# Kernel tuning notes

Hardware: AMD Instinct MI355X
Metric: run time of the kernel (lower is better)

Reference implementation:

```python
import jax, jax.numpy as jnp
import numpy as np

B = 2048          # graphs in dense batch
NPG = 64          # nodes per graph (molecules are small)
N = B * NPG       # 131072 total nodes
E = 524288        # directed edges, avg degree 4
D = 275           # dim_inner
L = 5             # layers_mp
NF = 9            # atom categorical features
V = 128           # per-feature vocab
BN_EPS = 1e-5


def setup_inputs() -> dict:
    key = jax.random.key(0)
    ks = jax.random.split(key, 8)
    return {
        "x_atoms": jax.random.randint(ks[0], (N, NF), 0, 119, dtype=jnp.int64),
        "edge_index": jax.random.randint(ks[1], (2, E), 0, N, dtype=jnp.int64),
        "atom_emb": jax.random.normal(ks[2], (NF, V, D), jnp.float32) * 0.1,
        "conv_W": jax.random.normal(ks[3], (L, D, D), jnp.float32) * (1.0 / np.sqrt(D)),
        "conv_b": jnp.zeros((L, D), jnp.float32),
        "bn_gamma": jnp.ones((L, D), jnp.float32),
        "bn_beta": jnp.zeros((L, D), jnp.float32),
        "post_W": jax.random.normal(ks[4], (D, D), jnp.float32) * (1.0 / np.sqrt(D)),
        "post_b": jnp.zeros((D,), jnp.float32),
    }


def reference(x_atoms, edge_index, atom_emb, conv_W, conv_b, bn_gamma, bn_beta, post_W, post_b):
    n = x_atoms.shape[0]
    # AtomEncoder: sum of per-feature embedding lookups -> [N, D]
    h = jax.vmap(lambda tab, idx: tab[idx], in_axes=(0, 1))(atom_emb, x_atoms).sum(0)

    # GCN normalization with self loops (shared across layers since graph is fixed)
    loops = jnp.arange(n, dtype=edge_index.dtype)
    row = jnp.concatenate([edge_index[0], loops])  # source
    col = jnp.concatenate([edge_index[1], loops])  # target (aggregation index)
    deg = jax.ops.segment_sum(jnp.ones_like(row, h.dtype), col, num_segments=n)
    dinv = jnp.where(deg > 0, jax.lax.rsqrt(jnp.maximum(deg, 1e-12)), 0.0)
    norm = dinv[row] * dinv[col]  # [E+N]

    for i in range(L):
        xw = h @ conv_W[i].T                                   # [N, D] linear (no bias yet)
        msg = norm[:, None] * xw[row]                          # gather + edge scaling
        agg = jax.ops.segment_sum(msg, col, num_segments=n) + conv_b[i]
        # BatchNorm1d (training-mode batch stats, biased variance)
        mu = agg.mean(axis=0)
        var = agg.var(axis=0)
        hbn = (agg - mu) * jax.lax.rsqrt(var + BN_EPS) * bn_gamma[i] + bn_beta[i]
        h = jax.nn.relu(hbn)

    # post_mp: single Linear (MLPNoAct, num_layers=1)
    h = h @ post_W.T + post_b

    # graph_preprocess -> dense batch [B, NPG, D], then pairwise dot-product decode
    hd = h.reshape(B, NPG, D)
    logits = jnp.einsum('bnd,bmd->bnm', hd, hd)[..., None]     # [B, NPG, NPG, 1]
    return logits
```

## Files before the change

kernel.cpp:

```cpp
#include <hip/hip_runtime.h>
#include <hip/hip_bf16.h>
#include <cstdint>

#define NN 131072
#define NE 524288
#define DIM 275
#define DP 288
#define NFEAT 9
#define NVOC 128
#define NLAY 5
#define NPG 64
#define NGRAPH 2048
#define BN_EPS 1e-5f
#define BK 32
#define NEPAD (NE + 3 * NN)
#define LDSE 1536

typedef unsigned short u16;
typedef __attribute__((ext_vector_type(8))) short s16x8;
typedef __attribute__((ext_vector_type(4))) float f32x4;

#define GLL16(g, l) __builtin_amdgcn_global_load_lds( \
    (const __attribute__((address_space(1))) unsigned int*)(g), \
    (__attribute__((address_space(3))) unsigned int*)(l), 16, 0, 0)

__device__ __forceinline__ float bf2f(u16 u) {
  union { unsigned int i; float f; } x; x.i = ((unsigned int)u) << 16; return x.f;
}
__device__ __forceinline__ u16 f2bf(float f) {
  union { float f; unsigned int i; } x; x.f = f;
  unsigned int r = x.i + 0x7fffu + ((x.i >> 16) & 1u);
  return (u16)(r >> 16);
}
__device__ __forceinline__ void acc4(float* a, uint2 m) {
  a[0] += bf2f((u16)m.x); a[1] += bf2f((u16)(m.x >> 16));
  a[2] += bf2f((u16)m.y); a[3] += bf2f((u16)(m.y >> 16));
}


__global__ void hist_kernel(const int* __restrict__ ei, int* __restrict__ cnt) {
  int e = blockIdx.x * 256 + threadIdx.x;
  if (e < NE) atomicAdd(&cnt[ei[NE + e]], 1);
}

__global__ void pad_dinv_kernel(const int* __restrict__ cnt, int* __restrict__ cnt_pad,
                                float* __restrict__ dinv) {
  int v = blockIdx.x * 256 + threadIdx.x;
  if (v < NN) {
    int c = cnt[v];
    cnt_pad[v] = (c + 3) & ~3;
    dinv[v] = rsqrtf(1.0f + (float)c);
  }
}

__global__ void scan_block_kernel(const int* __restrict__ in, int* __restrict__ out_ex,
                                  int* __restrict__ partials) {
  __shared__ int buf[2][1024];
  int t = threadIdx.x;
  int idx = blockIdx.x * 1024 + t;
  int v = in[idx];
  buf[0][t] = v;
  __syncthreads();
  int cur = 0;
  for (int off = 1; off < 1024; off <<= 1) {
    int x = buf[cur][t];
    if (t >= off) x += buf[cur][t - off];
    buf[cur ^ 1][t] = x;
    __syncthreads();
    cur ^= 1;
  }
  out_ex[idx] = buf[cur][t] - v;
  if (t == 1023) partials[blockIdx.x] = buf[cur][t];
}

__global__ void scan_partials_kernel(int* partials) {
  __shared__ int buf[2][128];
  int t = threadIdx.x;
  int v = partials[t];
  buf[0][t] = v;
  __syncthreads();
  int cur = 0;
  for (int off = 1; off < 128; off <<= 1) {
    int x = buf[cur][t];
    if (t >= off) x += buf[cur][t - off];
    buf[cur ^ 1][t] = x;
    __syncthreads();
    cur ^= 1;
  }
  partials[t] = buf[cur][t] - v;
}

__global__ void add_offsets_kernel(int* __restrict__ indptr, const int* __restrict__ partials,
                                   int* __restrict__ cursor, const int* __restrict__ cnt_pad) {
  int i = blockIdx.x * 256 + threadIdx.x;
  if (i < NN) {
    int v = indptr[i] + partials[i >> 10];
    indptr[i] = v;
    cursor[i] = v;
    if (i == NN - 1) indptr[NN] = v + cnt_pad[NN - 1];
  }
}

__global__ void fill_csr_kernel(const int* __restrict__ ei, int* __restrict__ cursor,
                                int* __restrict__ srcs) {
  int e = blockIdx.x * 256 + threadIdx.x;
  if (e < NE) {
    int c = ei[NE + e];
    int p = atomicAdd(&cursor[c], 1);
    srcs[p] = ei[e];
  }
}

__global__ void pad_fill_kernel(const int* __restrict__ cursor, const int* __restrict__ indptr,
                                int* __restrict__ srcs) {
  int v = blockIdx.x * 256 + threadIdx.x;
  if (v < NN) {
    int pe = indptr[v + 1];
    for (int p = cursor[v]; p < pe; ++p) srcs[p] = NN;
  }
}

__global__ void zrow_kernel(u16* __restrict__ P, u16* __restrict__ Q) {
  int i = threadIdx.x;
  if (i < DP) {
    P[(size_t)NN * DP + i] = 0;
    Q[(size_t)NN * DP + i] = 0;
  }
}

__global__ void wpad_kernel(const float* __restrict__ convW, const float* __restrict__ postW,
                            u16* __restrict__ Wp) {
  int i = blockIdx.x * 256 + threadIdx.x;
  const int total = 6 * 320 * DP;
  if (i >= total) return;
  int k = i % DP;
  int r = i / DP;
  int j = r % 320;
  int m = r / 320;
  float val = 0.f;
  if (j < DIM && k < DIM)
    val = (m < 5) ? convW[((size_t)m * DIM + j) * DIM + k] : postW[(size_t)j * DIM + k];
  int s = (j & 3) ^ ((j >> 2) & 3);
  int kout = (k & ~24) | (((((k >> 3) & 3)) ^ s) << 3);
  Wp[(size_t)r * DP + kout] = f2bf(val);
}


__global__ void embed_kernel(const int* __restrict__ xa, const float* __restrict__ emb,
                             u16* __restrict__ P) {
  int n = blockIdx.x;
  int idx[NFEAT];
#pragma unroll
  for (int f = 0; f < NFEAT; ++f) idx[f] = xa[n * NFEAT + f];
  for (int d = threadIdx.x; d < DP; d += 128) {
    float s = 0.f;
    if (d < DIM) {
#pragma unroll
      for (int f = 0; f < NFEAT; ++f) s += emb[((size_t)f * NVOC + idx[f]) * DIM + d];
    }
    P[(size_t)n * DP + d] = f2bf(s);
  }
}


__device__ __forceinline__ uint4 xform8s(uint4 r, const float* __restrict__ sc,
                                         const float* __restrict__ sh, int k) {
  union { uint4 u; u16 h[8]; } in, out;
  in.u = r;
#pragma unroll
  for (int j = 0; j < 8; ++j) {
    float x = fmaf(bf2f(in.h[j]), sc[k + j], sh[k + j]);
    out.h[j] = f2bf(fmaxf(x, 0.f));
  }
  return out.u;
}

__launch_bounds__(256)
__global__ void gemm_kernel(const u16* __restrict__ A, const u16* __restrict__ Wq,
                            u16* __restrict__ C,
                            const float* __restrict__ bn_sum, const float* __restrict__ bn_sq,
                            const float* __restrict__ gamma, const float* __restrict__ beta,
                            const float* __restrict__ rowscale, const float* __restrict__ colbias) {
  __shared__ __align__(16) u16 Asl[2][64 * BK];
  __shared__ __align__(16) u16 Bsl[2][288 * BK];
  __shared__ float scs[DP], shs[DP];
  const int tid = threadIdx.x, lane = tid & 63, wv = tid >> 6;
  const int wm = wv & 1, wn = wv >> 1;
  const int row0 = blockIdx.x * 64;
  const bool bn = (bn_sum != nullptr);

  for (int d = tid; d < DP; d += 256) {
    float sc = 1.f, sh = 0.f;
    if (bn) {
      if (d < DIM) {
        const float invN = 1.0f / (float)NN;
        float mu = bn_sum[d] * invN;
        float var = bn_sq[d] * invN - mu * mu;
        float rstd = rsqrtf(var + BN_EPS);
        sc = gamma[d] * rstd;
        sh = fmaf(-mu, sc, beta[d]);
      } else {
        sc = 0.f; sh = 0.f;
      }
    }
    scs[d] = sc; shs[d] = sh;
  }

  const int srow = tid >> 2, schk = tid & 3;
  const int swz = ((schk ^ (srow & 3) ^ ((srow >> 2) & 3)) << 3);
  const int awoff = srow * BK + swz;
  const u16* ag = A + (size_t)(row0 + srow) * DP + schk * 8;
  const int grow = lane >> 2, gchk = (lane & 3) * 8;

  const int fr = lane & 15, fs = lane >> 4;
  int aoff[2], boff[9];
#pragma unroll
  for (int i = 0; i < 2; ++i) {
    int r = wm * 32 + i * 16 + fr;
    aoff[i] = r * BK + ((fs ^ (r & 3) ^ ((r >> 2) & 3)) << 3);
  }
#pragma unroll
  for (int j = 0; j < 9; ++j) {
    int r = wn * 144 + j * 16 + fr;
    boff[j] = r * BK + ((fs ^ (r & 3) ^ ((r >> 2) & 3)) << 3);
  }

  for (int i = wv; i < 18; i += 4)
    GLL16(Wq + (size_t)(i * 16 + grow) * DP + gchk, &Bsl[0][i * 512]);
  uint4 ra = *(const uint4*)(ag);
  __syncthreads();
  if (bn) ra = xform8s(ra, scs, shs, schk * 8);
  *(uint4*)&Asl[0][awoff] = ra;
  __syncthreads();

  f32x4 acc0[9], acc1[9];
#pragma unroll
  for (int j = 0; j < 9; ++j) {
    acc0[j] = (f32x4){0.f, 0.f, 0.f, 0.f};
    acc1[j] = (f32x4){0.f, 0.f, 0.f, 0.f};
  }

#pragma unroll 1
  for (int s = 0; s < 9; ++s) {
    const int cur = s & 1;
    const bool more = (s < 8);
    uint4 na;
    if (more) {
      int k = (s + 1) * BK;
      for (int i = wv; i < 18; i += 4)
        GLL16(Wq + (size_t)(i * 16 + grow) * DP + k + gchk, &Bsl[cur ^ 1][i * 512]);
      na = *(const uint4*)(ag + k);
    }
    s16x8 af0 = *(const s16x8*)&Asl[cur][aoff[0]];
    s16x8 af1 = *(const s16x8*)&Asl[cur][aoff[1]];
#pragma unroll
    for (int j = 0; j < 9; ++j) {
      s16x8 bf = *(const s16x8*)&Bsl[cur][boff[j]];
      acc0[j] = __builtin_amdgcn_mfma_f32_16x16x32_bf16(af0, bf, acc0[j], 0, 0, 0);
      acc1[j] = __builtin_amdgcn_mfma_f32_16x16x32_bf16(af1, bf, acc1[j], 0, 0, 0);
    }
    if (more) {
      if (bn) na = xform8s(na, scs, shs, (s + 1) * BK + schk * 8);
      *(uint4*)&Asl[cur ^ 1][awoff] = na;
    }
    __syncthreads();
  }

#pragma unroll
  for (int i = 0; i < 2; ++i) {
    int gr0 = row0 + wm * 32 + i * 16 + fs * 4;
    float rs[4];
#pragma unroll
    for (int r = 0; r < 4; ++r) rs[r] = rowscale ? rowscale[gr0 + r] : 1.f;
#pragma unroll
    for (int j = 0; j < 9; ++j) {
      f32x4 av = i ? acc1[j] : acc0[j];
      int gc = wn * 144 + j * 16 + fr;
      float cb = (colbias && gc < DIM) ? colbias[gc] : 0.f;
#pragma unroll
      for (int r = 0; r < 4; ++r) {
        u16 o = (gc < DIM) ? f2bf(fmaf(av[r], rs[r], cb)) : (u16)0;
        C[(size_t)(gr0 + r) * DP + gc] = o;
      }
    }
  }
}


__launch_bounds__(256)
__global__ void spmm_kernel(const u16* __restrict__ X, u16* __restrict__ Y,
                            const int* __restrict__ indptr, const int* __restrict__ srcs,
                            const float* __restrict__ dinv, const float* __restrict__ bias,
                            float* __restrict__ bn_sum, float* __restrict__ bn_sq) {
  __shared__ float ls[DP], lq[DP];
  __shared__ int sptr[65];
  __shared__ __align__(16) int sidx[LDSE];
  int tid = threadIdx.x;
  for (int i = tid; i < DP; i += 256) { ls[i] = 0.f; lq[i] = 0.f; }
  int vb = blockIdx.x * 64;
  if (tid < 65) sptr[tid] = indptr[vb + tid];
  __syncthreads();
  int ebase = sptr[0];
  int ecnt = sptr[64] - ebase;
  const int* ip;
  if (ecnt <= LDSE) {
    for (int i = tid; i < ecnt; i += 256) sidx[i] = srcs[ebase + i];
    ip = sidx;
  } else {
    ip = srcs + ebase;
  }
  __syncthreads();

  int lane = tid & 63, wv = tid >> 6;
  int c0 = lane << 2;
  int lane2 = lane & 7;
  int c1 = 256 + (lane2 << 2);
  bool tl = lane < 16;
  bool loA = lane < 8;
  float bia[4], bib[4];
#pragma unroll
  for (int j = 0; j < 4; ++j) bia[j] = bias[c0 + j];
#pragma unroll
  for (int j = 0; j < 4; ++j) bib[j] = (tl && c1 + j < DIM) ? bias[c1 + j] : 0.f;
  float s0[4] = {}, q0[4] = {}, s1[4] = {}, q1[4] = {};

  for (int g = 0; g < 8; ++g) {
    int nA = wv * 16 + g;
    int nB = nA + 8;
    int ebA = sptr[nA] - ebase, neA = sptr[nA + 1] - sptr[nA];
    int ebB = sptr[nB] - ebase, neB = sptr[nB + 1] - sptr[nB];
    int nemax = neA > neB ? neA : neB;
    const u16* xA = X + (size_t)(vb + nA) * DP;
    const u16* xB = X + (size_t)(vb + nB) * DP;
    uint2 mA = *(const uint2*)(xA + c0);
    uint2 mB = *(const uint2*)(xB + c0);
    uint2 tS;
    if (tl) tS = *(const uint2*)((loA ? xA : xB) + c1);
    float A0[4] = {}, B0[4] = {}, C1[4] = {};
    acc4(A0, mA); acc4(B0, mB);
    if (tl) acc4(C1, tS);

    for (int e = 0; e < nemax; e += 4) {
      bool aA = e < neA, aB = e < neB;
      int oA = aA ? ebA + e : 0;
      int oB = aB ? ebB + e : 0;
      int4 i4a = *(const int4*)(ip + oA);
      int4 i4b = *(const int4*)(ip + oB);
      int ia[4], ib[4];
      ia[0] = aA ? i4a.x : NN; ia[1] = aA ? i4a.y : NN;
      ia[2] = aA ? i4a.z : NN; ia[3] = aA ? i4a.w : NN;
      ib[0] = aB ? i4b.x : NN; ib[1] = aB ? i4b.y : NN;
      ib[2] = aB ? i4b.z : NN; ib[3] = aB ? i4b.w : NN;
      const u16* pa[4]; const u16* pb[4];
#pragma unroll
      for (int j = 0; j < 4; ++j) {
        pa[j] = X + (size_t)ia[j] * DP;
        pb[j] = X + (size_t)ib[j] * DP;
      }
      uint2 ma[4], mb[4];
#pragma unroll
      for (int j = 0; j < 4; ++j) ma[j] = *(const uint2*)(pa[j] + c0);
#pragma unroll
      for (int j = 0; j < 4; ++j) mb[j] = *(const uint2*)(pb[j] + c0);
      uint2 tc[4];
      if (tl) {
#pragma unroll
        for (int j = 0; j < 4; ++j) tc[j] = *(const uint2*)((loA ? pa[j] : pb[j]) + c1);
      }
#pragma unroll
      for (int j = 0; j < 4; ++j) { acc4(A0, ma[j]); acc4(B0, mb[j]); }
      if (tl) {
#pragma unroll
        for (int j = 0; j < 4; ++j) acc4(C1, tc[j]);
      }
    }

    float dvA = dinv[vb + nA], dvB = dinv[vb + nB];
    u16* yA = Y + (size_t)(vb + nA) * DP;
    u16* yB = Y + (size_t)(vb + nB) * DP;
    float ya[4], yb[4];
#pragma unroll
    for (int j = 0; j < 4; ++j) {
      ya[j] = fmaf(dvA, A0[j], bia[j]);
      s0[j] += ya[j]; q0[j] += ya[j] * ya[j];
      yb[j] = fmaf(dvB, B0[j], bia[j]);
      s0[j] += yb[j]; q0[j] += yb[j] * yb[j];
    }
    uint2 wa, wb;
    wa.x = (unsigned)f2bf(ya[0]) | ((unsigned)f2bf(ya[1]) << 16);
    wa.y = (unsigned)f2bf(ya[2]) | ((unsigned)f2bf(ya[3]) << 16);
    wb.x = (unsigned)f2bf(yb[0]) | ((unsigned)f2bf(yb[1]) << 16);
    wb.y = (unsigned)f2bf(yb[2]) | ((unsigned)f2bf(yb[3]) << 16);
    *(uint2*)(yA + c0) = wa;
    *(uint2*)(yB + c0) = wb;
    if (tl) {
      float dvS = loA ? dvA : dvB;
      u16* yS = loA ? yA : yB;
      float z[4];
#pragma unroll
      for (int j = 0; j < 4; ++j) {
        z[j] = fmaf(dvS, C1[j], bib[j]);
        s1[j] += z[j]; q1[j] += z[j] * z[j];
      }
      uint2 w2;
      w2.x = (unsigned)f2bf(z[0]) | ((unsigned)f2bf(z[1]) << 16);
      w2.y = (unsigned)f2bf(z[2]) | ((unsigned)f2bf(z[3]) << 16);
      *(uint2*)(yS + c1) = w2;
    }
  }

#pragma unroll
  for (int j = 0; j < 4; ++j) { atomicAdd(&ls[c0 + j], s0[j]); atomicAdd(&lq[c0 + j], q0[j]); }
  if (tl) {
#pragma unroll
    for (int j = 0; j < 4; ++j) { atomicAdd(&ls[c1 + j], s1[j]); atomicAdd(&lq[c1 + j], q1[j]); }
  }
  __syncthreads();
  for (int i = tid; i < DP; i += 256) {
    atomicAdd(&bn_sum[i], ls[i]);
    atomicAdd(&bn_sq[i], lq[i]);
  }
}


__launch_bounds__(256)
__global__ void decode_kernel(const u16* __restrict__ H, float* __restrict__ out) {
  __shared__ __align__(16) u16 tile[4][2][NPG * BK];
  int tid = threadIdx.x, lane = tid & 63, wv = tid >> 6;
  int g = blockIdx.x * 4 + wv;
  const u16* Hg = H + (size_t)g * NPG * DP;
  const int ssl = lane & 3;
  int soff[4];
  const u16* sg[4];
#pragma unroll
  for (int i = 0; i < 4; ++i) {
    int r = (lane >> 2) + i * 16;
    soff[i] = r * BK + ((ssl ^ (r & 3) ^ ((r >> 2) & 3)) << 3);
    sg[i] = Hg + (size_t)r * DP + ssl * 8;
  }
  const int fr = lane & 15, fs = lane >> 4;
  const int fswz = ((fs ^ (fr & 3) ^ ((fr >> 2) & 3)) << 3);
  int foff[4];
#pragma unroll
  for (int i = 0; i < 4; ++i) foff[i] = (i * 16 + fr) * BK + fswz;

  u16* t0 = tile[wv][0];
  u16* t1 = tile[wv][1];
  uint4 rg[4];
#pragma unroll
  for (int i = 0; i < 4; ++i) rg[i] = *(const uint4*)(sg[i]);
#pragma unroll
  for (int i = 0; i < 4; ++i) *(uint4*)&t0[soff[i]] = rg[i];

  f32x4 acc[4][4];
#pragma unroll
  for (int i = 0; i < 4; ++i)
#pragma unroll
    for (int j = 0; j < 4; ++j) acc[i][j] = (f32x4){0.f, 0.f, 0.f, 0.f};

  for (int s = 0; s < DP / BK; ++s) {
    u16* cur = (s & 1) ? t1 : t0;
    u16* nxt = (s & 1) ? t0 : t1;
    const bool more = (s < DP / BK - 1);
    if (more) {
#pragma unroll
      for (int i = 0; i < 4; ++i) rg[i] = *(const uint4*)(sg[i] + (s + 1) * BK);
    }
    s16x8 af[4];
#pragma unroll
    for (int i = 0; i < 4; ++i) af[i] = *(const s16x8*)&cur[foff[i]];
#pragma unroll
    for (int i = 0; i < 4; ++i)
#pragma unroll
      for (int j = 0; j < 4; ++j)
        acc[i][j] = __builtin_amdgcn_mfma_f32_16x16x32_bf16(af[i], af[j], acc[i][j], 0, 0, 0);
    if (more) {
#pragma unroll
      for (int i = 0; i < 4; ++i) *(uint4*)&nxt[soff[i]] = rg[i];
    }
  }
  float* og = out + (size_t)g * NPG * NPG;
#pragma unroll
  for (int i = 0; i < 4; ++i) {
    int m0 = i * 16 + fs * 4;
#pragma unroll
    for (int j = 0; j < 4; ++j) {
      int n = j * 16 + fr;
#pragma unroll
      for (int r = 0; r < 4; ++r) og[(m0 + r) * NPG + n] = acc[i][j][r];
    }
  }
}


extern "C" void kernel_launch(void* const* d_in, const int* in_sizes, int n_in,
                              void* d_out, int out_size, void* d_ws, size_t ws_size,
                              hipStream_t stream) {
  const int* xa = (const int*)d_in[0];
  const int* ei = (const int*)d_in[1];
  const float* emb = (const float*)d_in[2];
  const float* convW = (const float*)d_in[3];
  const float* convB = (const float*)d_in[4];
  const float* gamma = (const float*)d_in[5];
  const float* beta = (const float*)d_in[6];
  const float* postW = (const float*)d_in[7];
  const float* postB = (const float*)d_in[8];
  float* out = (float*)d_out;

  char* w = (char*)d_ws;
  u16* P = (u16*)w;          w += (size_t)(NN + 1) * DP * sizeof(u16);
  u16* Q = (u16*)w;          w += (size_t)(NN + 1) * DP * sizeof(u16);
  u16* Wp = (u16*)w;         w += (size_t)6 * 320 * DP * sizeof(u16);
  float* dinv = (float*)w;   w += (size_t)NN * sizeof(float);
  int* cnt = (int*)w;        w += (size_t)NN * sizeof(int);
  int* cnt_pad = (int*)w;    w += (size_t)NN * sizeof(int);
  int* indptr = (int*)w;     w += (size_t)(NN + 64) * sizeof(int);
  int* cursor = (int*)w;     w += (size_t)NN * sizeof(int);
  int* srcs = (int*)w;       w += (size_t)NEPAD * sizeof(int);
  int* partials = (int*)w;   w += 256 * sizeof(int);
  float* bnstats = (float*)w; w += (size_t)NLAY * 2 * DP * sizeof(float);

  size_t need = (size_t)(w - (char*)d_ws);
  if (ws_size < need) return;

  hipMemsetAsync(cnt, 0, (size_t)NN * sizeof(int), stream);
  hipMemsetAsync(bnstats, 0, (size_t)NLAY * 2 * DP * sizeof(float), stream);
  hist_kernel<<<NE / 256, 256, 0, stream>>>(ei, cnt);
  pad_dinv_kernel<<<NN / 256, 256, 0, stream>>>(cnt, cnt_pad, dinv);
  scan_block_kernel<<<NN / 1024, 1024, 0, stream>>>(cnt_pad, indptr, partials);
  scan_partials_kernel<<<1, 128, 0, stream>>>(partials);
  add_offsets_kernel<<<NN / 256, 256, 0, stream>>>(indptr, partials, cursor, cnt_pad);
  fill_csr_kernel<<<NE / 256, 256, 0, stream>>>(ei, cursor, srcs);
  pad_fill_kernel<<<NN / 256, 256, 0, stream>>>(cursor, indptr, srcs);
  wpad_kernel<<<(6 * 320 * DP + 255) / 256, 256, 0, stream>>>(convW, postW, Wp);
  embed_kernel<<<NN, 128, 0, stream>>>(xa, emb, P);
  zrow_kernel<<<1, 288, 0, stream>>>(P, Q);

  for (int l = 0; l < NLAY; ++l) {
    const float* bs = l ? bnstats + (size_t)(l - 1) * 2 * DP : nullptr;
    gemm_kernel<<<NN / 64, 256, 0, stream>>>(
        P, Wp + (size_t)l * 320 * DP, Q,
        bs, bs ? bs + DP : nullptr,
        l ? gamma + (size_t)(l - 1) * DIM : nullptr,
        l ? beta + (size_t)(l - 1) * DIM : nullptr,
        dinv, nullptr);
    spmm_kernel<<<NN / 64, 256, 0, stream>>>(Q, P, indptr, srcs, dinv,
                                             convB + (size_t)l * DIM,
                                             bnstats + (size_t)l * 2 * DP,
                                             bnstats + (size_t)l * 2 * DP + DP);
  }

  const float* bs5 = bnstats + (size_t)4 * 2 * DP;
  gemm_kernel<<<NN / 64, 256, 0, stream>>>(
      P, Wp + (size_t)5 * 320 * DP, Q, bs5, bs5 + DP,
      gamma + (size_t)4 * DIM, beta + (size_t)4 * DIM, nullptr, postB);

  decode_kernel<<<NGRAPH / 4, 256, 0, stream>>>(Q, out);
}
```

Measured before the change: 996.6 us.

## Store node features in 16-column panels and split SpMM by panel

Node feature buffers move from row-major [N][288] to 18 column panels of [N+1][16], and every producer and consumer (embed, gemm, spmm, decode) is rewritten to match. The SpMM launches one block per (panel, 128-node group), so each panel's gathered rows fit a 4 MB working set that can stay cache-resident. The aim is to raise cache hit rates for the random neighbour gathers. The cost is that each edge index list is now read 18 times and each gather is only 4 bytes per lane, which may hurt coalescing.

```diff
diff --git a/kernel.cpp b/kernel.cpp
--- a/kernel.cpp
+++ b/kernel.cpp
@@ -6,6 +6,7 @@
 #define NE 524288
 #define DIM 275
 #define DP 288
+#define NPAN 18
 #define NFEAT 9
 #define NVOC 128
 #define NLAY 5
@@ -14,11 +15,13 @@
 #define BN_EPS 1e-5f
 #define BK 32
 #define NEPAD (NE + 3 * NN)
-#define LDSE 1536
+#define LDSE 1024
 
 typedef unsigned short u16;
 typedef __attribute__((ext_vector_type(8))) short s16x8;
 typedef __attribute__((ext_vector_type(4))) float f32x4;
+
+#define PS ((size_t)(NN + 1) * 16)
 
 #define GLL16(g, l) __builtin_amdgcn_global_load_lds( \
     (const __attribute__((address_space(1))) unsigned int*)(g), \
@@ -31,10 +34,6 @@
   union { float f; unsigned int i; } x; x.f = f;
   unsigned int r = x.i + 0x7fffu + ((x.i >> 16) & 1u);
   return (u16)(r >> 16);
-}
-__device__ __forceinline__ void acc4(float* a, uint2 m) {
-  a[0] += bf2f((u16)m.x); a[1] += bf2f((u16)(m.x >> 16));
-  a[2] += bf2f((u16)m.y); a[3] += bf2f((u16)(m.y >> 16));
 }
 
 
@@ -122,9 +121,10 @@
 
 __global__ void zrow_kernel(u16* __restrict__ P, u16* __restrict__ Q) {
   int i = threadIdx.x;
-  if (i < DP) {
-    P[(size_t)NN * DP + i] = 0;
-    Q[(size_t)NN * DP + i] = 0;
+  if (i < NPAN * 16) {
+    size_t off = (size_t)(i >> 4) * PS + (size_t)NN * 16 + (i & 15);
+    P[off] = 0;
+    Q[off] = 0;
   }
 }
 
@@ -158,7 +158,7 @@
 #pragma unroll
       for (int f = 0; f < NFEAT; ++f) s += emb[((size_t)f * NVOC + idx[f]) * DIM + d];
     }
-    P[(size_t)n * DP + d] = f2bf(s);
+    P[(size_t)(d >> 4) * PS + (size_t)n * 16 + (d & 15)] = f2bf(s);
   }
 }
 
@@ -209,7 +209,7 @@
   const int srow = tid >> 2, schk = tid & 3;
   const int swz = ((schk ^ (srow & 3) ^ ((srow >> 2) & 3)) << 3);
   const int awoff = srow * BK + swz;
-  const u16* ag = A + (size_t)(row0 + srow) * DP + schk * 8;
+  const u16* ag = A + (size_t)(schk >> 1) * PS + (size_t)(row0 + srow) * 16 + (schk & 1) * 8;
   const int grow = lane >> 2, gchk = (lane & 3) * 8;
 
   const int fr = lane & 15, fs = lane >> 4;
@@ -249,7 +249,7 @@
       int k = (s + 1) * BK;
       for (int i = wv; i < 18; i += 4)
         GLL16(Wq + (size_t)(i * 16 + grow) * DP + k + gchk, &Bsl[cur ^ 1][i * 512]);
-      na = *(const uint4*)(ag + k);
+      na = *(const uint4*)(ag + (size_t)(2 * (s + 1)) * PS);
     }
     s16x8 af0 = *(const s16x8*)&Asl[cur][aoff[0]];
     s16x8 af1 = *(const s16x8*)&Asl[cur][aoff[1]];
@@ -277,10 +277,11 @@
       f32x4 av = i ? acc1[j] : acc0[j];
       int gc = wn * 144 + j * 16 + fr;
       float cb = (colbias && gc < DIM) ? colbias[gc] : 0.f;
+      u16* cp = C + (size_t)(wn * 9 + j) * PS + (size_t)gr0 * 16 + fr;
 #pragma unroll
       for (int r = 0; r < 4; ++r) {
         u16 o = (gc < DIM) ? f2bf(fmaf(av[r], rs[r], cb)) : (u16)0;
-        C[(size_t)(gr0 + r) * DP + gc] = o;
+        cp[(size_t)r * 16] = o;
       }
     }
   }
@@ -292,16 +293,20 @@
                             const int* __restrict__ indptr, const int* __restrict__ srcs,
                             const float* __restrict__ dinv, const float* __restrict__ bias,
                             float* __restrict__ bn_sum, float* __restrict__ bn_sq) {
-  __shared__ float ls[DP], lq[DP];
-  __shared__ int sptr[65];
+  __shared__ int sptr[129];
   __shared__ __align__(16) int sidx[LDSE];
-  int tid = threadIdx.x;
-  for (int i = tid; i < DP; i += 256) { ls[i] = 0.f; lq[i] = 0.f; }
-  int vb = blockIdx.x * 64;
-  if (tid < 65) sptr[tid] = indptr[vb + tid];
+  __shared__ float ls[16], lq[16];
+  const int tid = threadIdx.x;
+  const int p = blockIdx.x >> 10;
+  const int g = blockIdx.x & 1023;
+  const int vb = g * 128;
+  const u16* Xp = X + (size_t)p * PS;
+  u16* Yp = Y + (size_t)p * PS;
+  if (tid < 129) sptr[tid] = indptr[vb + tid];
+  if (tid < 16) { ls[tid] = 0.f; lq[tid] = 0.f; }
   __syncthreads();
   int ebase = sptr[0];
-  int ecnt = sptr[64] - ebase;
+  int ecnt = sptr[128] - ebase;
   const int* ip;
   if (ecnt <= LDSE) {
     for (int i = tid; i < ecnt; i += 256) sidx[i] = srcs[ebase + i];
@@ -311,114 +316,64 @@
   }
   __syncthreads();
 
-  int lane = tid & 63, wv = tid >> 6;
-  int c0 = lane << 2;
-  int lane2 = lane & 7;
-  int c1 = 256 + (lane2 << 2);
-  bool tl = lane < 16;
-  bool loA = lane < 8;
-  float bia[4], bib[4];
-#pragma unroll
-  for (int j = 0; j < 4; ++j) bia[j] = bias[c0 + j];
-#pragma unroll
-  for (int j = 0; j < 4; ++j) bib[j] = (tl && c1 + j < DIM) ? bias[c1 + j] : 0.f;
-  float s0[4] = {}, q0[4] = {}, s1[4] = {}, q1[4] = {};
-
-  for (int g = 0; g < 8; ++g) {
-    int nA = wv * 16 + g;
-    int nB = nA + 8;
-    int ebA = sptr[nA] - ebase, neA = sptr[nA + 1] - sptr[nA];
-    int ebB = sptr[nB] - ebase, neB = sptr[nB + 1] - sptr[nB];
+  const int lane = tid & 63, wv = tid >> 6;
+  const int slot = lane >> 3;
+  const int cp = (lane & 7) << 1;
+  const int gc = p * 16 + cp;
+  float b0 = (gc < DIM) ? bias[gc] : 0.f;
+  float b1 = (gc + 1 < DIM) ? bias[gc + 1] : 0.f;
+  float s0 = 0.f, s1 = 0.f, q0 = 0.f, q1 = 0.f;
+
+  for (int h = 0; h < 2; ++h) {
+    int nlA = wv * 32 + h * 16 + slot;
+    int nlB = nlA + 8;
+    int nsA = vb + nlA, nsB = vb + nlB;
+    int ebA = sptr[nlA] - ebase, neA = sptr[nlA + 1] - sptr[nlA];
+    int ebB = sptr[nlB] - ebase, neB = sptr[nlB + 1] - sptr[nlB];
     int nemax = neA > neB ? neA : neB;
-    const u16* xA = X + (size_t)(vb + nA) * DP;
-    const u16* xB = X + (size_t)(vb + nB) * DP;
-    uint2 mA = *(const uint2*)(xA + c0);
-    uint2 mB = *(const uint2*)(xB + c0);
-    uint2 tS;
-    if (tl) tS = *(const uint2*)((loA ? xA : xB) + c1);
-    float A0[4] = {}, B0[4] = {}, C1[4] = {};
-    acc4(A0, mA); acc4(B0, mB);
-    if (tl) acc4(C1, tS);
-
+    unsigned mA = *(const unsigned*)(Xp + (size_t)nsA * 16 + cp);
+    unsigned mB = *(const unsigned*)(Xp + (size_t)nsB * 16 + cp);
+    float a0 = bf2f((u16)mA), a1 = bf2f((u16)(mA >> 16));
+    float c0 = bf2f((u16)mB), c1 = bf2f((u16)(mB >> 16));
     for (int e = 0; e < nemax; e += 4) {
       bool aA = e < neA, aB = e < neB;
       int oA = aA ? ebA + e : 0;
       int oB = aB ? ebB + e : 0;
-      int4 i4a = *(const int4*)(ip + oA);
-      int4 i4b = *(const int4*)(ip + oB);
       int ia[4], ib[4];
-      ia[0] = aA ? i4a.x : NN; ia[1] = aA ? i4a.y : NN;
-      ia[2] = aA ? i4a.z : NN; ia[3] = aA ? i4a.w : NN;
-      ib[0] = aB ? i4b.x : NN; ib[1] = aB ? i4b.y : NN;
-      ib[2] = aB ? i4b.z : NN; ib[3] = aB ? i4b.w : NN;
-      const u16* pa[4]; const u16* pb[4];
 #pragma unroll
       for (int j = 0; j < 4; ++j) {
-        pa[j] = X + (size_t)ia[j] * DP;
-        pb[j] = X + (size_t)ib[j] * DP;
+        int va = ip[oA + j], vx = ip[oB + j];
+        ia[j] = aA ? va : NN;
+        ib[j] = aB ? vx : NN;
       }
-      uint2 ma[4], mb[4];
-#pragma unroll
-      for (int j = 0; j < 4; ++j) ma[j] = *(const uint2*)(pa[j] + c0);
-#pragma unroll
-      for (int j = 0; j < 4; ++j) mb[j] = *(const uint2*)(pb[j] + c0);
-      uint2 tc[4];
-      if (tl) {
-#pragma unroll
-        for (int j = 0; j < 4; ++j) tc[j] = *(const uint2*)((loA ? pa[j] : pb[j]) + c1);
+      unsigned ga[4], gb[4];
+#pragma unroll
+      for (int j = 0; j < 4; ++j) ga[j] = *(const unsigned*)(Xp + (size_t)ia[j] * 16 + cp);
+#pragma unroll
+      for (int j = 0; j < 4; ++j) gb[j] = *(const unsigned*)(Xp + (size_t)ib[j] * 16 + cp);
+#pragma unroll
+      for (int j = 0; j < 4; ++j) {
+        a0 += bf2f((u16)ga[j]); a1 += bf2f((u16)(ga[j] >> 16));
+        c0 += bf2f((u16)gb[j]); c1 += bf2f((u16)(gb[j] >> 16));
       }
-#pragma unroll
-      for (int j = 0; j < 4; ++j) { acc4(A0, ma[j]); acc4(B0, mb[j]); }
-      if (tl) {
-#pragma unroll
-        for (int j = 0; j < 4; ++j) acc4(C1, tc[j]);
-      }
-    }
-
-    float dvA = dinv[vb + nA], dvB = dinv[vb + nB];
-    u16* yA = Y + (size_t)(vb + nA) * DP;
-    u16* yB = Y + (size_t)(vb + nB) * DP;
-    float ya[4], yb[4];
-#pragma unroll
-    for (int j = 0; j < 4; ++j) {
-      ya[j] = fmaf(dvA, A0[j], bia[j]);
-      s0[j] += ya[j]; q0[j] += ya[j] * ya[j];
-      yb[j] = fmaf(dvB, B0[j], bia[j]);
-      s0[j] += yb[j]; q0[j] += yb[j] * yb[j];
-    }
-    uint2 wa, wb;
-    wa.x = (unsigned)f2bf(ya[0]) | ((unsigned)f2bf(ya[1]) << 16);
-    wa.y = (unsigned)f2bf(ya[2]) | ((unsigned)f2bf(ya[3]) << 16);
-    wb.x = (unsigned)f2bf(yb[0]) | ((unsigned)f2bf(yb[1]) << 16);
-    wb.y = (unsigned)f2bf(yb[2]) | ((unsigned)f2bf(yb[3]) << 16);
-    *(uint2*)(yA + c0) = wa;
-    *(uint2*)(yB + c0) = wb;
-    if (tl) {
-      float dvS = loA ? dvA : dvB;
-      u16* yS = loA ? yA : yB;
-      float z[4];
-#pragma unroll
-      for (int j = 0; j < 4; ++j) {
-        z[j] = fmaf(dvS, C1[j], bib[j]);
-        s1[j] += z[j]; q1[j] += z[j] * z[j];
-      }
-      uint2 w2;
-      w2.x = (unsigned)f2bf(z[0]) | ((unsigned)f2bf(z[1]) << 16);
-      w2.y = (unsigned)f2bf(z[2]) | ((unsigned)f2bf(z[3]) << 16);
-      *(uint2*)(yS + c1) = w2;
-    }
-  }
-
-#pragma unroll
-  for (int j = 0; j < 4; ++j) { atomicAdd(&ls[c0 + j], s0[j]); atomicAdd(&lq[c0 + j], q0[j]); }
-  if (tl) {
-#pragma unroll
-    for (int j = 0; j < 4; ++j) { atomicAdd(&ls[c1 + j], s1[j]); atomicAdd(&lq[c1 + j], q1[j]); }
-  }
-  __syncthreads();
-  for (int i = tid; i < DP; i += 256) {
-    atomicAdd(&bn_sum[i], ls[i]);
-    atomicAdd(&bn_sq[i], lq[i]);
+    }
+    float dvA = dinv[nsA], dvB = dinv[nsB];
+    float yA0 = fmaf(dvA, a0, b0), yA1 = fmaf(dvA, a1, b1);
+    float yB0 = fmaf(dvB, c0, b0), yB1 = fmaf(dvB, c1, b1);
+    s0 += yA0 + yB0; q0 += yA0 * yA0 + yB0 * yB0;
+    s1 += yA1 + yB1; q1 += yA1 * yA1 + yB1 * yB1;
+    *(unsigned*)(Yp + (size_t)nsA * 16 + cp) =
+        (unsigned)f2bf(yA0) | ((unsigned)f2bf(yA1) << 16);
+    *(unsigned*)(Yp + (size_t)nsB * 16 + cp) =
+        (unsigned)f2bf(yB0) | ((unsigned)f2bf(yB1) << 16);
+  }
+
+  atomicAdd(&ls[cp], s0); atomicAdd(&ls[cp + 1], s1);
+  atomicAdd(&lq[cp], q0); atomicAdd(&lq[cp + 1], q1);
+  __syncthreads();
+  if (tid < 16) {
+    atomicAdd(&bn_sum[p * 16 + tid], ls[tid]);
+    atomicAdd(&bn_sq[p * 16 + tid], lq[tid]);
   }
 }
 
@@ -428,7 +383,6 @@
   __shared__ __align__(16) u16 tile[4][2][NPG * BK];
   int tid = threadIdx.x, lane = tid & 63, wv = tid >> 6;
   int g = blockIdx.x * 4 + wv;
-  const u16* Hg = H + (size_t)g * NPG * DP;
   const int ssl = lane & 3;
   int soff[4];
   const u16* sg[4];
@@ -436,7 +390,7 @@
   for (int i = 0; i < 4; ++i) {
     int r = (lane >> 2) + i * 16;
     soff[i] = r * BK + ((ssl ^ (r & 3) ^ ((r >> 2) & 3)) << 3);
-    sg[i] = Hg + (size_t)r * DP + ssl * 8;
+    sg[i] = H + (size_t)(ssl >> 1) * PS + (size_t)(g * NPG + r) * 16 + (ssl & 1) * 8;
   }
   const int fr = lane & 15, fs = lane >> 4;
   const int fswz = ((fs ^ (fr & 3) ^ ((fr >> 2) & 3)) << 3);
@@ -464,7 +418,8 @@
     const bool more = (s < DP / BK - 1);
     if (more) {
 #pragma unroll
-      for (int i = 0; i < 4; ++i) rg[i] = *(const uint4*)(sg[i] + (s + 1) * BK);
+      for (int i = 0; i < 4; ++i)
+        rg[i] = *(const uint4*)(sg[i] + (size_t)(2 * (s + 1)) * PS);
     }
     s16x8 af[4];
 #pragma unroll
@@ -544,10 +499,9 @@
         l ? gamma + (size_t)(l - 1) * DIM : nullptr,
         l ? beta + (size_t)(l - 1) * DIM : nullptr,
         dinv, nullptr);
-    spmm_kernel<<<NN / 64, 256, 0, stream>>>(Q, P, indptr, srcs, dinv,
-                                             convB + (size_t)l * DIM,
-                                             bnstats + (size_t)l * 2 * DP,
-                                             bnstats + (size_t)l * 2 * DP + DP);
+    spmm_kernel<<<NPAN * (NN / 128), 256, 0, stream>>>(
+        Q, P, indptr, srcs, dinv, convB + (size_t)l * DIM,
+        bnstats + (size_t)l * 2 * DP, bnstats + (size_t)l * 2 * DP + DP);
   }
 
   const float* bs5 = bnstats + (size_t)4 * 2 * DP;
```

Result: slower. 1.327 ms (+33.2%).

## Pre-pack weights in MFMA fragment order and load B directly to registers

Applied to the files above, without the earlier changes.

The weight matrices are repacked once into MFMA B-fragment order so each lane loads its 16-byte fragment straight from global memory (L2-resident) into registers, removing the shared-memory B tiles and global_load_lds staging. A tiles are now staged per wave in private LDS buffers, so the per-k-step block-wide __syncthreads is dropped. Launch bounds request 3 blocks per SM to raise occupancy now that LDS use is smaller. The trade-off is that every wave reissues global loads for the weights, which adds L2 traffic and exposes global latency inside the k loop.

```diff
diff --git a/kernel.cpp b/kernel.cpp
--- a/kernel.cpp
+++ b/kernel.cpp
@@ -15,14 +15,11 @@
 #define BK 32
 #define NEPAD (NE + 3 * NN)
 #define LDSE 1536
+#define WELEM (18 * 9 * 64 * 8)
 
 typedef unsigned short u16;
 typedef __attribute__((ext_vector_type(8))) short s16x8;
 typedef __attribute__((ext_vector_type(4))) float f32x4;
-
-#define GLL16(g, l) __builtin_amdgcn_global_load_lds( \
-    (const __attribute__((address_space(1))) unsigned int*)(g), \
-    (__attribute__((address_space(3))) unsigned int*)(l), 16, 0, 0)
 
 __device__ __forceinline__ float bf2f(u16 u) {
   union { unsigned int i; float f; } x; x.i = ((unsigned int)u) << 16; return x.f;
@@ -129,20 +126,22 @@
 }
 
 __global__ void wpad_kernel(const float* __restrict__ convW, const float* __restrict__ postW,
-                            u16* __restrict__ Wp) {
+                            u16* __restrict__ Wr) {
   int i = blockIdx.x * 256 + threadIdx.x;
-  const int total = 6 * 320 * DP;
+  const int total = 6 * WELEM;
   if (i >= total) return;
-  int k = i % DP;
-  int r = i / DP;
-  int j = r % 320;
-  int m = r / 320;
+  int e = i & 7;
+  int l = (i >> 3) & 63;
+  int rest = i >> 9;
+  int s = rest % 9; rest /= 9;
+  int jt = rest % 18;
+  int m = rest / 18;
+  int col = jt * 16 + (l & 15);
+  int k = s * 32 + (l >> 4) * 8 + e;
   float val = 0.f;
-  if (j < DIM && k < DIM)
-    val = (m < 5) ? convW[((size_t)m * DIM + j) * DIM + k] : postW[(size_t)j * DIM + k];
-  int s = (j & 3) ^ ((j >> 2) & 3);
-  int kout = (k & ~24) | (((((k >> 3) & 3)) ^ s) << 3);
-  Wp[(size_t)r * DP + kout] = f2bf(val);
+  if (col < DIM && k < DIM)
+    val = (m < 5) ? convW[((size_t)m * DIM + col) * DIM + k] : postW[(size_t)col * DIM + k];
+  Wr[i] = f2bf(val);
 }
 
 
@@ -163,26 +162,13 @@
 }
 
 
-__device__ __forceinline__ uint4 xform8s(uint4 r, const float* __restrict__ sc,
-                                         const float* __restrict__ sh, int k) {
-  union { uint4 u; u16 h[8]; } in, out;
-  in.u = r;
-#pragma unroll
-  for (int j = 0; j < 8; ++j) {
-    float x = fmaf(bf2f(in.h[j]), sc[k + j], sh[k + j]);
-    out.h[j] = f2bf(fmaxf(x, 0.f));
-  }
-  return out.u;
-}
-
-__launch_bounds__(256)
-__global__ void gemm_kernel(const u16* __restrict__ A, const u16* __restrict__ Wq,
+__launch_bounds__(256, 3)
+__global__ void gemm_kernel(const u16* __restrict__ A, const u16* __restrict__ Wr,
                             u16* __restrict__ C,
                             const float* __restrict__ bn_sum, const float* __restrict__ bn_sq,
                             const float* __restrict__ gamma, const float* __restrict__ beta,
                             const float* __restrict__ rowscale, const float* __restrict__ colbias) {
-  __shared__ __align__(16) u16 Asl[2][64 * BK];
-  __shared__ __align__(16) u16 Bsl[2][288 * BK];
+  __shared__ __align__(16) u16 Awp[4][2][32 * 32];
   __shared__ float scs[DP], shs[DP];
   const int tid = threadIdx.x, lane = tid & 63, wv = tid >> 6;
   const int wm = wv & 1, wn = wv >> 1;
@@ -206,32 +192,44 @@
     scs[d] = sc; shs[d] = sh;
   }
 
-  const int srow = tid >> 2, schk = tid & 3;
-  const int swz = ((schk ^ (srow & 3) ^ ((srow >> 2) & 3)) << 3);
-  const int awoff = srow * BK + swz;
-  const u16* ag = A + (size_t)(row0 + srow) * DP + schk * 8;
-  const int grow = lane >> 2, gchk = (lane & 3) * 8;
-
+  const int sr0 = lane >> 2, sch = lane & 3;
+  const int wp0 = sr0 * 32 + ((sch ^ (sr0 & 3)) << 3);
+  const int sr1 = 16 + sr0;
+  const int wp1 = sr1 * 32 + ((sch ^ (sr1 & 3)) << 3);
+  const u16* ag = A + (size_t)(row0 + wm * 32) * DP + sch * 8;
+  const u16* ag0 = ag + (size_t)sr0 * DP;
+  const u16* ag1 = ag + (size_t)sr1 * DP;
   const int fr = lane & 15, fs = lane >> 4;
-  int aoff[2], boff[9];
-#pragma unroll
-  for (int i = 0; i < 2; ++i) {
-    int r = wm * 32 + i * 16 + fr;
-    aoff[i] = r * BK + ((fs ^ (r & 3) ^ ((r >> 2) & 3)) << 3);
-  }
-#pragma unroll
-  for (int j = 0; j < 9; ++j) {
-    int r = wn * 144 + j * 16 + fr;
-    boff[j] = r * BK + ((fs ^ (r & 3) ^ ((r >> 2) & 3)) << 3);
-  }
-
-  for (int i = wv; i < 18; i += 4)
-    GLL16(Wq + (size_t)(i * 16 + grow) * DP + gchk, &Bsl[0][i * 512]);
-  uint4 ra = *(const uint4*)(ag);
+  const int ar0 = fr, ar1 = 16 + fr;
+  const int af0o = ar0 * 32 + (((fs) ^ (ar0 & 3)) << 3);
+  const int af1o = ar1 * 32 + (((fs) ^ (ar1 & 3)) << 3);
+  const u16* bg = Wr + ((size_t)(wn * 9) * 9 * 64 + lane) * 8;
+
   __syncthreads();
-  if (bn) ra = xform8s(ra, scs, shs, schk * 8);
-  *(uint4*)&Asl[0][awoff] = ra;
-  __syncthreads();
+
+  {
+    uint4 a0 = *(const uint4*)(ag0);
+    uint4 a1 = *(const uint4*)(ag1);
+    if (bn) {
+      int k = sch * 8;
+      float4 c0 = *(const float4*)&scs[k], c1 = *(const float4*)&scs[k + 4];
+      float4 h0 = *(const float4*)&shs[k], h1 = *(const float4*)&shs[k + 4];
+      union { uint4 u; u16 h[8]; } in0, in1, o0, o1;
+      in0.u = a0; in1.u = a1;
+      const float* cc = (const float*)&c0;
+      float sc[8] = {c0.x, c0.y, c0.z, c0.w, c1.x, c1.y, c1.z, c1.w};
+      float sh[8] = {h0.x, h0.y, h0.z, h0.w, h1.x, h1.y, h1.z, h1.w};
+      (void)cc;
+#pragma unroll
+      for (int j = 0; j < 8; ++j) {
+        o0.h[j] = f2bf(fmaxf(fmaf(bf2f(in0.h[j]), sc[j], sh[j]), 0.f));
+        o1.h[j] = f2bf(fmaxf(fmaf(bf2f(in1.h[j]), sc[j], sh[j]), 0.f));
+      }
+      a0 = o0.u; a1 = o1.u;
+    }
+    *(uint4*)&Awp[wv][0][wp0] = a0;
+    *(uint4*)&Awp[wv][0][wp1] = a1;
+  }
 
   f32x4 acc0[9], acc1[9];
 #pragma unroll
@@ -244,26 +242,43 @@
   for (int s = 0; s < 9; ++s) {
     const int cur = s & 1;
     const bool more = (s < 8);
-    uint4 na;
+    uint4 braw[9];
+#pragma unroll
+    for (int j = 0; j < 9; ++j)
+      braw[j] = *(const uint4*)(bg + (size_t)(j * 9 + s) * 64 * 8);
+    uint4 na0, na1;
     if (more) {
       int k = (s + 1) * BK;
-      for (int i = wv; i < 18; i += 4)
-        GLL16(Wq + (size_t)(i * 16 + grow) * DP + k + gchk, &Bsl[cur ^ 1][i * 512]);
-      na = *(const uint4*)(ag + k);
-    }
-    s16x8 af0 = *(const s16x8*)&Asl[cur][aoff[0]];
-    s16x8 af1 = *(const s16x8*)&Asl[cur][aoff[1]];
+      na0 = *(const uint4*)(ag0 + k);
+      na1 = *(const uint4*)(ag1 + k);
+    }
+    s16x8 af0 = *(const s16x8*)&Awp[wv][cur][af0o];
+    s16x8 af1 = *(const s16x8*)&Awp[wv][cur][af1o];
 #pragma unroll
     for (int j = 0; j < 9; ++j) {
-      s16x8 bf = *(const s16x8*)&Bsl[cur][boff[j]];
-      acc0[j] = __builtin_amdgcn_mfma_f32_16x16x32_bf16(af0, bf, acc0[j], 0, 0, 0);
-      acc1[j] = __builtin_amdgcn_mfma_f32_16x16x32_bf16(af1, bf, acc1[j], 0, 0, 0);
+      union { uint4 u; s16x8 v; } cb; cb.u = braw[j];
+      acc0[j] = __builtin_amdgcn_mfma_f32_16x16x32_bf16(af0, cb.v, acc0[j], 0, 0, 0);
+      acc1[j] = __builtin_amdgcn_mfma_f32_16x16x32_bf16(af1, cb.v, acc1[j], 0, 0, 0);
     }
     if (more) {
-      if (bn) na = xform8s(na, scs, shs, (s + 1) * BK + schk * 8);
-      *(uint4*)&Asl[cur ^ 1][awoff] = na;
-    }
-    __syncthreads();
+      if (bn) {
+        int k = (s + 1) * BK + sch * 8;
+        float4 c0 = *(const float4*)&scs[k], c1 = *(const float4*)&scs[k + 4];
+        float4 h0 = *(const float4*)&shs[k], h1 = *(const float4*)&shs[k + 4];
+        float sc[8] = {c0.x, c0.y, c0.z, c0.w, c1.x, c1.y, c1.z, c1.w};
+        float sh[8] = {h0.x, h0.y, h0.z, h0.w, h1.x, h1.y, h1.z, h1.w};
+        union { uint4 u; u16 h[8]; } in0, in1, o0, o1;
+        in0.u = na0; in1.u = na1;
+#pragma unroll
+        for (int j = 0; j < 8; ++j) {
+          o0.h[j] = f2bf(fmaxf(fmaf(bf2f(in0.h[j]), sc[j], sh[j]), 0.f));
+          o1.h[j] = f2bf(fmaxf(fmaf(bf2f(in1.h[j]), sc[j], sh[j]), 0.f));
+        }
+        na0 = o0.u; na1 = o1.u;
+      }
+      *(uint4*)&Awp[wv][cur ^ 1][wp0] = na0;
+      *(uint4*)&Awp[wv][cur ^ 1][wp1] = na1;
+    }
   }
 
 #pragma unroll
@@ -510,7 +525,7 @@
   char* w = (char*)d_ws;
   u16* P = (u16*)w;          w += (size_t)(NN + 1) * DP * sizeof(u16);
   u16* Q = (u16*)w;          w += (size_t)(NN + 1) * DP * sizeof(u16);
-  u16* Wp = (u16*)w;         w += (size_t)6 * 320 * DP * sizeof(u16);
+  u16* Wr = (u16*)w;         w += (size_t)6 * WELEM * sizeof(u16);
   float* dinv = (float*)w;   w += (size_t)NN * sizeof(float);
   int* cnt = (int*)w;        w += (size_t)NN * sizeof(int);
   int* cnt_pad = (int*)w;    w += (size_t)NN * sizeof(int);
@@ -532,14 +547,14 @@
   add_offsets_kernel<<<NN / 256, 256, 0, stream>>>(indptr, partials, cursor, cnt_pad);
   fill_csr_kernel<<<NE / 256, 256, 0, stream>>>(ei, cursor, srcs);
   pad_fill_kernel<<<NN / 256, 256, 0, stream>>>(cursor, indptr, srcs);
-  wpad_kernel<<<(6 * 320 * DP + 255) / 256, 256, 0, stream>>>(convW, postW, Wp);
+  wpad_kernel<<<(6 * WELEM + 255) / 256, 256, 0, stream>>>(convW, postW, Wr);
   embed_kernel<<<NN, 128, 0, stream>>>(xa, emb, P);
   zrow_kernel<<<1, 288, 0, stream>>>(P, Q);
 
   for (int l = 0; l < NLAY; ++l) {
     const float* bs = l ? bnstats + (size_t)(l - 1) * 2 * DP : nullptr;
     gemm_kernel<<<NN / 64, 256, 0, stream>>>(
-        P, Wp + (size_t)l * 320 * DP, Q,
+        P, Wr + (size_t)l * WELEM, Q,
         bs, bs ? bs + DP : nullptr,
         l ? gamma + (size_t)(l - 1) * DIM : nullptr,
         l ? beta + (size_t)(l - 1) * DIM : nullptr,
@@ -552,7 +567,7 @@
 
   const float* bs5 = bnstats + (size_t)4 * 2 * DP;
   gemm_kernel<<<NN / 64, 256, 0, stream>>>(
-      P, Wp + (size_t)5 * 320 * DP, Q, bs5, bs5 + DP,
+      P, Wr + (size_t)5 * WELEM, Q, bs5, bs5 + DP,
       gamma + (size_t)4 * DIM, beta + (size_t)4 * DIM, nullptr, postB);
 
   decode_kernel<<<NGRAPH / 4, 256, 0, stream>>>(Q, out);
```

New measurement: 974.0 us. 1.02x faster.
